# Performance work log

Hardware: AMD Instinct MI355X
Metric: run time of the kernel (lower is better)

Reference implementation:

```python
import jax, jax.numpy as jnp
import numpy as np

E = 2048        # embed_dim
HQ = 32         # num_query_heads
HKV = 8         # num_kv_heads
HD = E // HQ    # head_dim = 64
G = HQ // HKV   # queries per kv head = 4
B, T = 2, 2048


def setup_inputs() -> dict:
    key = jax.random.key(0)
    kx, kq, kkv, ko = jax.random.split(key, 4)
    s = 1.0 / np.sqrt(E)
    x = jax.random.normal(kx, (B, T, E), dtype=jnp.float32)
    Wq = jax.random.normal(kq, (E, E), dtype=jnp.float32) * s          # torch Linear weight (out,in)
    Wkv = jax.random.normal(kkv, (2 * HKV * HD, E), dtype=jnp.float32) * s
    Wo = jax.random.normal(ko, (E, E), dtype=jnp.float32) * s
    return {"x": x, "Wq": Wq, "Wkv": Wkv, "Wo": Wo}


def reference(x, Wq, Wkv, Wo):
    Bx, Tx, C = x.shape
    scale = 1.0 / np.sqrt(HD)
    # projections (torch Linear: y = x @ W.T)
    q = x @ Wq.T                                   # (B,T,E)
    kv = x @ Wkv.T                                 # (B,T,2*HKV*HD)
    k, v = jnp.split(kv, 2, axis=-1)               # each (B,T,HKV*HD)
    # grouped layout: q -> (B,HKV,G,T,HD); k,v -> (B,HKV,T,HD)
    q = q.reshape(Bx, Tx, HKV, G, HD).transpose(0, 2, 3, 1, 4)
    k = k.reshape(Bx, Tx, HKV, HD).transpose(0, 2, 1, 3)
    v = v.reshape(Bx, Tx, HKV, HD).transpose(0, 2, 1, 3)
    # scores: equivalent to repeat_interleave of K over query-head groups
    att = jnp.einsum('bhgtd,bhsd->bhgts', q, k) * scale   # (B,HKV,G,T,T)
    causal = jnp.triu(jnp.ones((Tx, Tx), dtype=bool), k=1)
    att = jnp.where(causal, -jnp.inf, att)
    att = jax.nn.softmax(att, axis=-1)
    out = jnp.einsum('bhgts,bhsd->bhgtd', att, v)          # (B,HKV,G,T,HD)
    out = out.transpose(0, 3, 1, 2, 4).reshape(Bx, Tx, C)  # (B,T,E)
    return out @ Wo.T
```

## Files before the change

kernel.cpp:

```cpp
#include <hip/hip_runtime.h>
#include <hip/hip_bf16.h>
#include <math.h>

#define GQA_B   2
#define GQA_T   2048
#define GQA_E   2048
#define GQA_HQ  32
#define GQA_HKV 8
#define GQA_HD  64
#define GQA_EKV 1024
#define GQA_M   (GQA_B * GQA_T)

typedef short  bf16x8 __attribute__((ext_vector_type(8)));
typedef float  f32x4  __attribute__((ext_vector_type(4)));

__device__ __forceinline__ ushort f2b(float f) {
  union { float f; unsigned u; } c; c.f = f;
  unsigned u = c.u;
  u += 0x7fffu + ((u >> 16) & 1u);
  return (ushort)(u >> 16);
}

__global__ __launch_bounds__(256) void cvt_f32_bf16(
    const float* __restrict__ src, ushort* __restrict__ dst, int n4) {
  int i = blockIdx.x * blockDim.x + threadIdx.x;
  const int stride = gridDim.x * blockDim.x;
  for (; i < n4; i += stride) {
    float4 v = *(const float4*)(src + (size_t)i * 4);
    ushort4 o;
    o.x = f2b(v.x); o.y = f2b(v.y); o.z = f2b(v.z); o.w = f2b(v.w);
    *(ushort4*)(dst + (size_t)i * 4) = o;
  }
}

__device__ __forceinline__ void store_out(ushort* p, float v) { *p = f2b(v); }
__device__ __forceinline__ void store_out(float* p, float v)  { *p = v; }

template <typename CT>
__global__ __launch_bounds__(256) void gemm_nt_bf16(
    const ushort* __restrict__ A, const ushort* __restrict__ B,
    CT* __restrict__ C, int M, int N, int K) {
  __shared__ __align__(16) ushort As[128 * 40];
  __shared__ __align__(16) ushort Bs[128 * 40];
  const int tid = threadIdx.x;
  const int l  = tid & 63;
  const int w  = tid >> 6;
  const int lm = l & 15;
  const int lg = l >> 4;
  const int wm = w & 1;
  const int wn = w >> 1;
  const int bm = blockIdx.y * 128;
  const int bn = blockIdx.x * 128;

  const int srow = tid >> 2;
  const int scol = (tid & 3) * 8;
  const ushort* Ag = A + (size_t)(bm + srow) * K + scol;
  const ushort* Bg = B + (size_t)(bn + srow) * K + scol;

  f32x4 acc[4][4];
#pragma unroll
  for (int i = 0; i < 4; ++i)
#pragma unroll
    for (int j = 0; j < 4; ++j)
#pragma unroll
      for (int r = 0; r < 4; ++r) acc[i][j][r] = 0.f;

  for (int k0 = 0; k0 < K; k0 += 32) {
    int4 a0 = *(const int4*)(Ag + k0);
    int4 a1 = *(const int4*)(Ag + (size_t)64 * K + k0);
    int4 b0 = *(const int4*)(Bg + k0);
    int4 b1 = *(const int4*)(Bg + (size_t)64 * K + k0);
    __syncthreads();
    *(int4*)(As + srow * 40 + scol)        = a0;
    *(int4*)(As + (srow + 64) * 40 + scol) = a1;
    *(int4*)(Bs + srow * 40 + scol)        = b0;
    *(int4*)(Bs + (srow + 64) * 40 + scol) = b1;
    __syncthreads();

    bf16x8 af[4], bfr[4];
#pragma unroll
    for (int mf = 0; mf < 4; ++mf)
      af[mf] = *(const bf16x8*)(As + (wm * 64 + mf * 16 + lm) * 40 + lg * 8);
#pragma unroll
    for (int nf = 0; nf < 4; ++nf)
      bfr[nf] = *(const bf16x8*)(Bs + (wn * 64 + nf * 16 + lm) * 40 + lg * 8);
#pragma unroll
    for (int mf = 0; mf < 4; ++mf)
#pragma unroll
      for (int nf = 0; nf < 4; ++nf)
        acc[mf][nf] = __builtin_amdgcn_mfma_f32_16x16x32_bf16(
            af[mf], bfr[nf], acc[mf][nf], 0, 0, 0);
  }

#pragma unroll
  for (int mf = 0; mf < 4; ++mf)
#pragma unroll
    for (int nf = 0; nf < 4; ++nf)
#pragma unroll
      for (int r = 0; r < 4; ++r) {
        const int row = bm + wm * 64 + mf * 16 + lg * 4 + r;
        const int col = bn + wn * 64 + nf * 16 + lm;
        store_out(C + (size_t)row * N + col, acc[mf][nf][r]);
      }
}

__global__ __launch_bounds__(256) void gqa_attn_mfma(
    const ushort* __restrict__ Q, const ushort* __restrict__ KV,
    ushort* __restrict__ Oat) {
  const int T = GQA_T, EQ = GQA_E, EKV = GQA_EKV;
  const int qt0 = blockIdx.x * 64;
  const int hq  = blockIdx.y;
  const int b   = blockIdx.z;
  const int hkv = hq >> 2;

  __shared__ __align__(16) ushort Ks[64 * 64];
  __shared__ __align__(16) ushort Vt[64 * 64];
  __shared__ __align__(16) ushort Ps[4 * 16 * 64];

  const int tid = threadIdx.x;
  const int w  = tid >> 6;
  const int l  = tid & 63;
  const int lm = l & 15;
  const int lg = l >> 4;

  const size_t qrow = ((size_t)b * T + qt0 + 16 * w + lm) * EQ + hq * 64;
  const bf16x8 qa0 = *(const bf16x8*)(Q + qrow + lg * 8);
  const bf16x8 qa1 = *(const bf16x8*)(Q + qrow + 32 + lg * 8);

  f32x4 oacc[4];
#pragma unroll
  for (int nd = 0; nd < 4; ++nd)
#pragma unroll
    for (int r = 0; r < 4; ++r) oacc[nd][r] = 0.f;
  float mrow[4], lrow[4];
#pragma unroll
  for (int r = 0; r < 4; ++r) { mrow[r] = -INFINITY; lrow[r] = 0.f; }

  const float scale = 0.125f;
  const size_t kvbase = (size_t)b * T * EKV + hkv * 64;

  const int kf_key = tid >> 3;
  const int kf_d   = (tid & 7) * 8;

  char* KsB = (char*)Ks;
  char* VtB = (char*)Vt;
  char* PsB = (char*)Ps + w * 2048;

  const int nt = blockIdx.x + 1;
  for (int t = 0; t < nt; ++t) {
    const int s0 = t * 64;
    int4 kr0 = *(const int4*)(KV + kvbase + (size_t)(s0 + kf_key) * EKV + kf_d);
    int4 kr1 = *(const int4*)(KV + kvbase + (size_t)(s0 + 32 + kf_key) * EKV + kf_d);
    int4 vr0 = *(const int4*)(KV + kvbase + 512 + (size_t)(s0 + l) * EKV + w * 8);
    int4 vr1 = *(const int4*)(KV + kvbase + 512 + (size_t)(s0 + l) * EKV + 32 + w * 8);
    __syncthreads();
    *(int4*)(KsB + kf_key * 128 + ((kf_d * 2) ^ ((kf_key & 7) << 4))) = kr0;
    *(int4*)(KsB + (kf_key + 32) * 128 + ((kf_d * 2) ^ ((kf_key & 7) << 4))) = kr1;
    {
      union { int4 v; ushort u[8]; } a, bq;
      a.v = vr0; bq.v = vr1;
#pragma unroll
      for (int j = 0; j < 8; ++j) {
        const int d0 = w * 8 + j;
        *(ushort*)(VtB + d0 * 128 + ((2 * l) ^ ((d0 & 7) << 4))) = a.u[j];
        const int d1 = 32 + w * 8 + j;
        *(ushort*)(VtB + d1 * 128 + ((2 * l) ^ ((d1 & 7) << 4))) = bq.u[j];
      }
    }
    __syncthreads();

    f32x4 sacc[4];
#pragma unroll
    for (int nf = 0; nf < 4; ++nf)
#pragma unroll
      for (int r = 0; r < 4; ++r) sacc[nf][r] = 0.f;
#pragma unroll
    for (int nf = 0; nf < 4; ++nf) {
      const int krow = nf * 16 + lm;
      const int swz = (krow & 7) << 4;
      bf16x8 kb0 = *(const bf16x8*)(KsB + krow * 128 + ((lg * 16) ^ swz));
      bf16x8 kb1 = *(const bf16x8*)(KsB + krow * 128 + ((64 + lg * 16) ^ swz));
      sacc[nf] = __builtin_amdgcn_mfma_f32_16x16x32_bf16(qa0, kb0, sacc[nf], 0, 0, 0);
      sacc[nf] = __builtin_amdgcn_mfma_f32_16x16x32_bf16(qa1, kb1, sacc[nf], 0, 0, 0);
    }

    const int qg = qt0 + 16 * w + lg * 4;
    if (t == nt - 1) {
#pragma unroll
      for (int nf = 0; nf < 4; ++nf)
#pragma unroll
        for (int r = 0; r < 4; ++r) {
          const int sg = s0 + nf * 16 + lm;
          const float sv = sacc[nf][r] * scale;
          sacc[nf][r] = (sg <= qg + r) ? sv : -INFINITY;
        }
    } else {
#pragma unroll
      for (int nf = 0; nf < 4; ++nf)
#pragma unroll
        for (int r = 0; r < 4; ++r) sacc[nf][r] *= scale;
    }

#pragma unroll
    for (int r = 0; r < 4; ++r) {
      float m4 = fmaxf(fmaxf(sacc[0][r], sacc[1][r]), fmaxf(sacc[2][r], sacc[3][r]));
      m4 = fmaxf(m4, __shfl_xor(m4, 1, 16));
      m4 = fmaxf(m4, __shfl_xor(m4, 2, 16));
      m4 = fmaxf(m4, __shfl_xor(m4, 4, 16));
      m4 = fmaxf(m4, __shfl_xor(m4, 8, 16));
      const float mnew = fmaxf(mrow[r], m4);
      const float alpha = __expf(mrow[r] - mnew);
      mrow[r] = mnew;
      float ssum = 0.f;
#pragma unroll
      for (int nf = 0; nf < 4; ++nf) {
        const float p = __expf(sacc[nf][r] - mnew);
        sacc[nf][r] = p;
        ssum += p;
      }
      ssum += __shfl_xor(ssum, 1, 16);
      ssum += __shfl_xor(ssum, 2, 16);
      ssum += __shfl_xor(ssum, 4, 16);
      ssum += __shfl_xor(ssum, 8, 16);
      lrow[r] = lrow[r] * alpha + ssum;
#pragma unroll
      for (int nd = 0; nd < 4; ++nd) oacc[nd][r] *= alpha;
    }

#pragma unroll
    for (int nf = 0; nf < 4; ++nf)
#pragma unroll
      for (int r = 0; r < 4; ++r) {
        const int q = lg * 4 + r;
        const int keyb = 2 * (nf * 16 + lm);
        *(ushort*)(PsB + q * 128 + (keyb ^ ((q & 7) << 4))) = f2b(sacc[nf][r]);
      }

    {
      const char* pw = PsB + lm * 128;
      const int pswz = (lm & 7) << 4;
      bf16x8 pa0 = *(const bf16x8*)(pw + ((lg * 16) ^ pswz));
      bf16x8 pa1 = *(const bf16x8*)(pw + ((64 + lg * 16) ^ pswz));
#pragma unroll
      for (int nd = 0; nd < 4; ++nd) {
        const int vrow = nd * 16 + lm;
        const int vswz = (vrow & 7) << 4;
        bf16x8 vb0 = *(const bf16x8*)(VtB + vrow * 128 + ((lg * 16) ^ vswz));
        bf16x8 vb1 = *(const bf16x8*)(VtB + vrow * 128 + ((64 + lg * 16) ^ vswz));
        oacc[nd] = __builtin_amdgcn_mfma_f32_16x16x32_bf16(pa0, vb0, oacc[nd], 0, 0, 0);
        oacc[nd] = __builtin_amdgcn_mfma_f32_16x16x32_bf16(pa1, vb1, oacc[nd], 0, 0, 0);
      }
    }
  }

  float inv[4];
#pragma unroll
  for (int r = 0; r < 4; ++r) inv[r] = 1.f / lrow[r];
  const size_t ob = ((size_t)b * T + qt0 + 16 * w + lg * 4) * EQ + hq * 64 + lm;
#pragma unroll
  for (int nd = 0; nd < 4; ++nd)
#pragma unroll
    for (int r = 0; r < 4; ++r)
      Oat[ob + (size_t)r * EQ + nd * 16] = f2b(oacc[nd][r] * inv[r]);
}

extern "C" void kernel_launch(void* const* d_in, const int* in_sizes, int n_in,
                              void* d_out, int out_size, void* d_ws, size_t ws_size,
                              hipStream_t stream) {
  const float* x   = (const float*)d_in[0];
  const float* Wq  = (const float*)d_in[1];
  const float* Wkv = (const float*)d_in[2];
  const float* Wo  = (const float*)d_in[3];
  float* out = (float*)d_out;

  ushort* xb   = (ushort*)d_ws;
  ushort* wqb  = xb   + (size_t)GQA_M * GQA_E;
  ushort* wkvb = wqb  + (size_t)GQA_E * GQA_E;
  ushort* wob  = wkvb + (size_t)GQA_EKV * GQA_E;
  ushort* qb   = wob  + (size_t)GQA_E * GQA_E;
  ushort* kvb  = qb   + (size_t)GQA_M * GQA_E;
  ushort* attb = kvb  + (size_t)GQA_M * GQA_EKV;

  cvt_f32_bf16<<<2048, 256, 0, stream>>>(x,   xb,   GQA_M * GQA_E / 4);
  cvt_f32_bf16<<<1024, 256, 0, stream>>>(Wq,  wqb,  GQA_E * GQA_E / 4);
  cvt_f32_bf16<<<512,  256, 0, stream>>>(Wkv, wkvb, GQA_EKV * GQA_E / 4);
  cvt_f32_bf16<<<1024, 256, 0, stream>>>(Wo,  wob,  GQA_E * GQA_E / 4);

  gemm_nt_bf16<ushort><<<dim3(GQA_E / 128, GQA_M / 128), 256, 0, stream>>>(
      xb, wqb, qb, GQA_M, GQA_E, GQA_E);
  gemm_nt_bf16<ushort><<<dim3(GQA_EKV / 128, GQA_M / 128), 256, 0, stream>>>(
      xb, wkvb, kvb, GQA_M, GQA_EKV, GQA_E);
  gqa_attn_mfma<<<dim3(GQA_T / 64, GQA_HQ, GQA_B), 256, 0, stream>>>(
      qb, kvb, attb);
  gemm_nt_bf16<float><<<dim3(GQA_E / 128, GQA_M / 128), 256, 0, stream>>>(
      attb, wob, out, GQA_M, GQA_E, GQA_E);
}
```

Baseline: 502.3 us.

## Use direct global-to-LDS loads, transposed score MFMA, exp2 softmax, reversed tile order

The GEMM now stages A/B tiles with global_load_lds, which writes straight into unpadded LDS. This drops the register round trip and one barrier per K step, but the tiles lose their padding and may hit LDS bank conflicts. The attention kernel also loads K with global_load_lds using a pre-swizzled source, and computes S^T so each lane owns one query row. That cuts the row max/sum shuffles and lets P be stored packed. It also switches to exp2 with a folded log2e scale and launches the longest causal query tiles first to balance the load.

New measurement: 460.7 us. -8.3%, faster.

```diff
diff --git a/kernel.cpp b/kernel.cpp
--- a/kernel.cpp
+++ b/kernel.cpp
@@ -13,6 +13,11 @@
 
 typedef short  bf16x8 __attribute__((ext_vector_type(8)));
 typedef float  f32x4  __attribute__((ext_vector_type(4)));
+
+#define GLDS16(gsrc, ldst)                                                 \
+  __builtin_amdgcn_global_load_lds(                                       \
+      (const __attribute__((address_space(1))) void*)(gsrc),              \
+      (__attribute__((address_space(3))) void*)(ldst), 16, 0, 0)
 
 __device__ __forceinline__ ushort f2b(float f) {
   union { float f; unsigned u; } c; c.f = f;
@@ -40,8 +45,8 @@
 __global__ __launch_bounds__(256) void gemm_nt_bf16(
     const ushort* __restrict__ A, const ushort* __restrict__ B,
     CT* __restrict__ C, int M, int N, int K) {
-  __shared__ __align__(16) ushort As[128 * 40];
-  __shared__ __align__(16) ushort Bs[128 * 40];
+  __shared__ __align__(16) ushort As[128 * 32];
+  __shared__ __align__(16) ushort Bs[128 * 32];
   const int tid = threadIdx.x;
   const int l  = tid & 63;
   const int w  = tid >> 6;
@@ -52,10 +57,12 @@
   const int bm = blockIdx.y * 128;
   const int bn = blockIdx.x * 128;
 
-  const int srow = tid >> 2;
-  const int scol = (tid & 3) * 8;
+  const int srow = w * 32 + (l >> 2);
+  const int scol = (l & 3) * 8;
   const ushort* Ag = A + (size_t)(bm + srow) * K + scol;
   const ushort* Bg = B + (size_t)(bn + srow) * K + scol;
+  char* ldsA = (char*)As + w * 2048;
+  char* ldsB = (char*)Bs + w * 2048;
 
   f32x4 acc[4][4];
 #pragma unroll
@@ -66,30 +73,26 @@
       for (int r = 0; r < 4; ++r) acc[i][j][r] = 0.f;
 
   for (int k0 = 0; k0 < K; k0 += 32) {
-    int4 a0 = *(const int4*)(Ag + k0);
-    int4 a1 = *(const int4*)(Ag + (size_t)64 * K + k0);
-    int4 b0 = *(const int4*)(Bg + k0);
-    int4 b1 = *(const int4*)(Bg + (size_t)64 * K + k0);
+    GLDS16(Ag + k0,                  ldsA);
+    GLDS16(Ag + (size_t)16 * K + k0, ldsA + 1024);
+    GLDS16(Bg + k0,                  ldsB);
+    GLDS16(Bg + (size_t)16 * K + k0, ldsB + 1024);
     __syncthreads();
-    *(int4*)(As + srow * 40 + scol)        = a0;
-    *(int4*)(As + (srow + 64) * 40 + scol) = a1;
-    *(int4*)(Bs + srow * 40 + scol)        = b0;
-    *(int4*)(Bs + (srow + 64) * 40 + scol) = b1;
-    __syncthreads();
 
     bf16x8 af[4], bfr[4];
 #pragma unroll
     for (int mf = 0; mf < 4; ++mf)
-      af[mf] = *(const bf16x8*)(As + (wm * 64 + mf * 16 + lm) * 40 + lg * 8);
-#pragma unroll
-    for (int nf = 0; nf < 4; ++nf)
-      bfr[nf] = *(const bf16x8*)(Bs + (wn * 64 + nf * 16 + lm) * 40 + lg * 8);
+      af[mf] = *(const bf16x8*)(As + (wm * 64 + mf * 16 + lm) * 32 + lg * 8);
+#pragma unroll
+    for (int nf = 0; nf < 4; ++nf)
+      bfr[nf] = *(const bf16x8*)(Bs + (wn * 64 + nf * 16 + lm) * 32 + lg * 8);
 #pragma unroll
     for (int mf = 0; mf < 4; ++mf)
 #pragma unroll
       for (int nf = 0; nf < 4; ++nf)
         acc[mf][nf] = __builtin_amdgcn_mfma_f32_16x16x32_bf16(
             af[mf], bfr[nf], acc[mf][nf], 0, 0, 0);
+    __syncthreads();
   }
 
 #pragma unroll
@@ -108,7 +111,8 @@
     const ushort* __restrict__ Q, const ushort* __restrict__ KV,
     ushort* __restrict__ Oat) {
   const int T = GQA_T, EQ = GQA_E, EKV = GQA_EKV;
-  const int qt0 = blockIdx.x * 64;
+  const int qt  = (int)gridDim.x - 1 - (int)blockIdx.x;
+  const int qt0 = qt * 64;
   const int hq  = blockIdx.y;
   const int b   = blockIdx.z;
   const int hkv = hq >> 2;
@@ -132,30 +136,29 @@
   for (int nd = 0; nd < 4; ++nd)
 #pragma unroll
     for (int r = 0; r < 4; ++r) oacc[nd][r] = 0.f;
-  float mrow[4], lrow[4];
-#pragma unroll
-  for (int r = 0; r < 4; ++r) { mrow[r] = -INFINITY; lrow[r] = 0.f; }
-
-  const float scale = 0.125f;
+  float m2 = -INFINITY, lsum = 0.f;
+  const float SCL2 = 0.125f * 1.44269504088896f;
+
   const size_t kvbase = (size_t)b * T * EKV + hkv * 64;
 
-  const int kf_key = tid >> 3;
-  const int kf_d   = (tid & 7) * 8;
-
+  const int k_key  = w * 8 + (l >> 3);
+  const int k_srcd = (((l & 7) ^ (l >> 3)) * 8);
   char* KsB = (char*)Ks;
   char* VtB = (char*)Vt;
   char* PsB = (char*)Ps + w * 2048;
-
-  const int nt = blockIdx.x + 1;
+  char* ldsK0 = KsB + w * 1024;
+  char* ldsK1 = KsB + (4 + w) * 1024;
+  const int pswz = (lm & 7) << 4;
+
+  const int nt = qt + 1;
   for (int t = 0; t < nt; ++t) {
     const int s0 = t * 64;
-    int4 kr0 = *(const int4*)(KV + kvbase + (size_t)(s0 + kf_key) * EKV + kf_d);
-    int4 kr1 = *(const int4*)(KV + kvbase + (size_t)(s0 + 32 + kf_key) * EKV + kf_d);
+    const ushort* kg0 = KV + kvbase + (size_t)(s0 + k_key) * EKV + k_srcd;
     int4 vr0 = *(const int4*)(KV + kvbase + 512 + (size_t)(s0 + l) * EKV + w * 8);
     int4 vr1 = *(const int4*)(KV + kvbase + 512 + (size_t)(s0 + l) * EKV + 32 + w * 8);
     __syncthreads();
-    *(int4*)(KsB + kf_key * 128 + ((kf_d * 2) ^ ((kf_key & 7) << 4))) = kr0;
-    *(int4*)(KsB + (kf_key + 32) * 128 + ((kf_d * 2) ^ ((kf_key & 7) << 4))) = kr1;
+    GLDS16(kg0,                       ldsK0);
+    GLDS16(kg0 + (size_t)32 * EKV,    ldsK1);
     {
       union { int4 v; ushort u[8]; } a, bq;
       a.v = vr0; bq.v = vr1;
@@ -180,67 +183,69 @@
       const int swz = (krow & 7) << 4;
       bf16x8 kb0 = *(const bf16x8*)(KsB + krow * 128 + ((lg * 16) ^ swz));
       bf16x8 kb1 = *(const bf16x8*)(KsB + krow * 128 + ((64 + lg * 16) ^ swz));
-      sacc[nf] = __builtin_amdgcn_mfma_f32_16x16x32_bf16(qa0, kb0, sacc[nf], 0, 0, 0);
-      sacc[nf] = __builtin_amdgcn_mfma_f32_16x16x32_bf16(qa1, kb1, sacc[nf], 0, 0, 0);
-    }
-
-    const int qg = qt0 + 16 * w + lg * 4;
+      sacc[nf] = __builtin_amdgcn_mfma_f32_16x16x32_bf16(kb0, qa0, sacc[nf], 0, 0, 0);
+      sacc[nf] = __builtin_amdgcn_mfma_f32_16x16x32_bf16(kb1, qa1, sacc[nf], 0, 0, 0);
+    }
+
+    const int qg = qt0 + 16 * w + lm;
     if (t == nt - 1) {
 #pragma unroll
       for (int nf = 0; nf < 4; ++nf)
 #pragma unroll
         for (int r = 0; r < 4; ++r) {
-          const int sg = s0 + nf * 16 + lm;
-          const float sv = sacc[nf][r] * scale;
-          sacc[nf][r] = (sg <= qg + r) ? sv : -INFINITY;
+          const int sg = s0 + nf * 16 + lg * 4 + r;
+          const float sv = sacc[nf][r] * SCL2;
+          sacc[nf][r] = (sg <= qg) ? sv : -INFINITY;
         }
     } else {
 #pragma unroll
       for (int nf = 0; nf < 4; ++nf)
 #pragma unroll
-        for (int r = 0; r < 4; ++r) sacc[nf][r] *= scale;
-    }
-
-#pragma unroll
-    for (int r = 0; r < 4; ++r) {
-      float m4 = fmaxf(fmaxf(sacc[0][r], sacc[1][r]), fmaxf(sacc[2][r], sacc[3][r]));
-      m4 = fmaxf(m4, __shfl_xor(m4, 1, 16));
-      m4 = fmaxf(m4, __shfl_xor(m4, 2, 16));
-      m4 = fmaxf(m4, __shfl_xor(m4, 4, 16));
-      m4 = fmaxf(m4, __shfl_xor(m4, 8, 16));
-      const float mnew = fmaxf(mrow[r], m4);
-      const float alpha = __expf(mrow[r] - mnew);
-      mrow[r] = mnew;
-      float ssum = 0.f;
-#pragma unroll
-      for (int nf = 0; nf < 4; ++nf) {
-        const float p = __expf(sacc[nf][r] - mnew);
+        for (int r = 0; r < 4; ++r) sacc[nf][r] *= SCL2;
+    }
+
+    float mt = -INFINITY;
+#pragma unroll
+    for (int nf = 0; nf < 4; ++nf)
+#pragma unroll
+      for (int r = 0; r < 4; ++r) mt = fmaxf(mt, sacc[nf][r]);
+    mt = fmaxf(mt, __shfl_xor(mt, 16));
+    mt = fmaxf(mt, __shfl_xor(mt, 32));
+    const float mnew = fmaxf(m2, mt);
+    const float alpha = exp2f(m2 - mnew);
+    m2 = mnew;
+    float ssum = 0.f;
+#pragma unroll
+    for (int nf = 0; nf < 4; ++nf)
+#pragma unroll
+      for (int r = 0; r < 4; ++r) {
+        const float p = exp2f(sacc[nf][r] - mnew);
         sacc[nf][r] = p;
         ssum += p;
       }
-      ssum += __shfl_xor(ssum, 1, 16);
-      ssum += __shfl_xor(ssum, 2, 16);
-      ssum += __shfl_xor(ssum, 4, 16);
-      ssum += __shfl_xor(ssum, 8, 16);
-      lrow[r] = lrow[r] * alpha + ssum;
-#pragma unroll
-      for (int nd = 0; nd < 4; ++nd) oacc[nd][r] *= alpha;
-    }
-
-#pragma unroll
-    for (int nf = 0; nf < 4; ++nf)
-#pragma unroll
-      for (int r = 0; r < 4; ++r) {
-        const int q = lg * 4 + r;
-        const int keyb = 2 * (nf * 16 + lm);
-        *(ushort*)(PsB + q * 128 + (keyb ^ ((q & 7) << 4))) = f2b(sacc[nf][r]);
-      }
+    ssum += __shfl_xor(ssum, 16);
+    ssum += __shfl_xor(ssum, 32);
+    lsum = lsum * alpha + ssum;
+
+    float ar[4];
+#pragma unroll
+    for (int r = 0; r < 4; ++r) ar[r] = __shfl(alpha, lg * 4 + r);
+#pragma unroll
+    for (int nd = 0; nd < 4; ++nd)
+#pragma unroll
+      for (int r = 0; r < 4; ++r) oacc[nd][r] *= ar[r];
+
+#pragma unroll
+    for (int nf = 0; nf < 4; ++nf) {
+      union { uint2 v; __hip_bfloat162 h[2]; } pk;
+      pk.h[0] = __float22bfloat162_rn(make_float2(sacc[nf][0], sacc[nf][1]));
+      pk.h[1] = __float22bfloat162_rn(make_float2(sacc[nf][2], sacc[nf][3]));
+      *(uint2*)(PsB + lm * 128 + ((nf * 32 + lg * 8) ^ pswz)) = pk.v;
+    }
 
     {
-      const char* pw = PsB + lm * 128;
-      const int pswz = (lm & 7) << 4;
-      bf16x8 pa0 = *(const bf16x8*)(pw + ((lg * 16) ^ pswz));
-      bf16x8 pa1 = *(const bf16x8*)(pw + ((64 + lg * 16) ^ pswz));
+      bf16x8 pa0 = *(const bf16x8*)(PsB + lm * 128 + ((lg * 16) ^ pswz));
+      bf16x8 pa1 = *(const bf16x8*)(PsB + lm * 128 + ((64 + lg * 16) ^ pswz));
 #pragma unroll
       for (int nd = 0; nd < 4; ++nd) {
         const int vrow = nd * 16 + lm;
@@ -253,15 +258,16 @@
     }
   }
 
-  float inv[4];
-#pragma unroll
-  for (int r = 0; r < 4; ++r) inv[r] = 1.f / lrow[r];
+  const float inv_own = 1.f / lsum;
+  float ir[4];
+#pragma unroll
+  for (int r = 0; r < 4; ++r) ir[r] = __shfl(inv_own, lg * 4 + r);
   const size_t ob = ((size_t)b * T + qt0 + 16 * w + lg * 4) * EQ + hq * 64 + lm;
 #pragma unroll
   for (int nd = 0; nd < 4; ++nd)
 #pragma unroll
     for (int r = 0; r < 4; ++r)
-      Oat[ob + (size_t)r * EQ + nd * 16] = f2b(oacc[nd][r] * inv[r]);
+      Oat[ob + (size_t)r * EQ + nd * 16] = f2b(oacc[nd][r] * ir[r]);
 }
 
 extern "C" void kernel_launch(void* const* d_in, const int* in_sizes, int n_in,
```
